# Kernel optimization log

Hardware: AMD Instinct MI355X
Metric: run time of the kernel (lower is better)

## Reference

```python
import jax, jax.numpy as jnp
import numpy as np

N_EMBED = 1024
N_HEAD = 16


def setup_inputs() -> dict:
    key = jax.random.key(0)
    k1, k2, k3 = jax.random.split(key, 3)
    B, T, C = 4, 2048, N_EMBED
    x = jax.random.normal(k1, (B, T, C), dtype=jnp.float32)
    # Linear weights stored as [in, out] so forward is x @ W
    scale = 1.0 / np.sqrt(C)
    W_attn = jax.random.normal(k2, (C, 3 * C), dtype=jnp.float32) * scale
    W_proj = jax.random.normal(k3, (C, C), dtype=jnp.float32) * scale
    return {"x": x, "W_attn": W_attn, "W_proj": W_proj}


def reference(x, W_attn, W_proj):
    B, T, C = x.shape
    H = N_HEAD
    D = C // H
    qkv = x @ W_attn  # [B, T, 3C]
    q, k, v = jnp.split(qkv, 3, axis=-1)
    # [B, H, T, D]
    q = q.reshape(B, T, H, D).transpose(0, 2, 1, 3)
    k = k.reshape(B, T, H, D).transpose(0, 2, 1, 3)
    v = v.reshape(B, T, H, D).transpose(0, 2, 1, 3)
    scores = jnp.einsum('bhqd,bhkd->bhqk', q, k) * (1.0 / np.sqrt(D))
    causal = jnp.tril(jnp.ones((T, T), dtype=bool))
    scores = jnp.where(causal, scores, -jnp.inf)
    attn = jax.nn.softmax(scores, axis=-1)
    y = jnp.einsum('bhqk,bhkd->bhqd', attn, v)  # [B, H, T, D]
    y = y.transpose(0, 2, 1, 3).reshape(B, T, C)
    return y @ W_proj
```

## Files before the change

kernel.cpp:

```cpp
#include <hip/hip_runtime.h>

using bf16x8 = __attribute__((ext_vector_type(8))) __bf16;
using f32x4  = __attribute__((ext_vector_type(4))) float;
using f32x16 = __attribute__((ext_vector_type(16))) float;

__device__ __forceinline__ unsigned short f2bf(float f) {
  unsigned u = __builtin_bit_cast(unsigned, f);
  u += 0x7fffu + ((u >> 16) & 1u);
  return (unsigned short)(u >> 16);
}

__device__ __forceinline__ unsigned cvt_pk_bf16(float lo, float hi) {
  unsigned r;
  asm("v_cvt_pk_bf16_f32 %0, %1, %2" : "=v"(r) : "v"(lo), "v"(hi));
  return r;
}

__device__ __forceinline__ void permswap(unsigned &a, unsigned &b) {
  asm("v_permlane32_swap_b32 %0, %1" : "+v"(a), "+v"(b));
}

__device__ __forceinline__ void gload_lds16(const void* g, void* l) {
  __builtin_amdgcn_global_load_lds((const __attribute__((address_space(1))) void*)g,
                                   (__attribute__((address_space(3))) void*)l, 16, 0, 0);
}

__global__ void prep_kernel(const float* __restrict__ x, unsigned short* __restrict__ xb,
                            const float* __restrict__ Wa, unsigned short* __restrict__ WaT,
                            const float* __restrict__ Wp, unsigned short* __restrict__ WpT) {
  __shared__ float tile[32][33];
  const int bid = blockIdx.x;
  const int tid = threadIdx.x;
  if (bid < 8192) {
    int i = (bid * 256 + tid) * 4;
    float4 f = *(const float4*)(x + i);
    ushort4 o;
    o.x = f2bf(f.x); o.y = f2bf(f.y); o.z = f2bf(f.z); o.w = f2bf(f.w);
    *(ushort4*)(xb + i) = o;
    return;
  }
  const float* W; unsigned short* WT; int N, tb;
  if (bid < 11264) { W = Wa; WT = WaT; N = 3072; tb = bid - 8192; }
  else             { W = Wp; WT = WpT; N = 1024; tb = bid - 11264; }
  const int nt = N >> 5;
  const int n0 = (tb % nt) * 32, k0 = (tb / nt) * 32;
  const int tx = tid & 31, ty = tid >> 5;
  #pragma unroll
  for (int i = 0; i < 32; i += 8)
    tile[ty + i][tx] = W[(size_t)(k0 + ty + i) * N + (n0 + tx)];
  __syncthreads();
  #pragma unroll
  for (int i = 0; i < 32; i += 8)
    WT[(size_t)(n0 + ty + i) * 1024 + (k0 + tx)] = f2bf(tile[tx][ty + i]);
}

template <int MODE>
__global__ __launch_bounds__(256, 2)
void gemm_bf16(const unsigned short* __restrict__ A,
               const unsigned short* __restrict__ BT,
               float* __restrict__ Cout, int K,
               unsigned short* __restrict__ q_out,
               unsigned short* __restrict__ k_out,
               unsigned short* __restrict__ v_out, int N) {
  __shared__ alignas(16) char smem[32768];
  char* As = smem;
  char* Bs = smem + 16384;
  const int tid = threadIdx.x;
  const int lane = tid & 63, w = tid >> 6;
  const int wm = w >> 1, wn = w & 1;
  const int l15 = lane & 15, l4 = lane >> 4;
  const int bm = blockIdx.y, bn = blockIdx.x;

  f32x4 acc[4][4] = {};

  for (int kt = 0; kt < K; kt += 64) {
    #pragma unroll
    for (int i = 0; i < 4; i++) {
      int row = i * 32 + w * 8 + (lane >> 3);
      int sc = (lane & 7) ^ (row & 7);
      gload_lds16(A + (size_t)(bm * 128 + row) * K + kt + sc * 8, As + i * 4096 + w * 1024);
      gload_lds16(BT + (size_t)(bn * 128 + row) * K + kt + sc * 8, Bs + i * 4096 + w * 1024);
    }
    __syncthreads();
    #pragma unroll
    for (int kk = 0; kk < 2; kk++) {
      bf16x8 af[4], bfr[4];
      #pragma unroll
      for (int mc = 0; mc < 4; mc++) {
        int row = wm * 64 + mc * 16 + l15;
        af[mc] = *(const bf16x8*)(As + row * 128 + (((kk * 4 + l4) ^ (row & 7)) << 4));
      }
      #pragma unroll
      for (int nc = 0; nc < 4; nc++) {
        int row = wn * 64 + nc * 16 + l15;
        bfr[nc] = *(const bf16x8*)(Bs + row * 128 + (((kk * 4 + l4) ^ (row & 7)) << 4));
      }
      #pragma unroll
      for (int mc = 0; mc < 4; mc++)
        #pragma unroll
        for (int nc = 0; nc < 4; nc++)
          acc[mc][nc] = __builtin_amdgcn_mfma_f32_16x16x32_bf16(af[mc], bfr[nc], acc[mc][nc], 0, 0, 0);
    }
    __syncthreads();
  }

  if (MODE == 0 && bn >= 16) {
    unsigned short* tt = (unsigned short*)smem;
    #pragma unroll
    for (int mc = 0; mc < 4; mc++)
      #pragma unroll
      for (int nc = 0; nc < 4; nc++)
        #pragma unroll
        for (int r = 0; r < 4; r++) {
          int ml = wm * 64 + mc * 16 + l4 * 4 + r;
          int nl = wn * 64 + nc * 16 + l15;
          tt[nl * 128 + (ml ^ ((nl & 7) << 3))] = f2bf(acc[mc][nc][r]);
        }
    __syncthreads();
    const int b_ = bm >> 4;
    const int t0 = (bm & 15) * 128;
    const int mm = (tid & 15) * 8;
    #pragma unroll
    for (int it = 0; it < 8; it++) {
      int nl = it * 16 + (tid >> 4);
      int n = bn * 128 + nl;
      int h = (n >> 6) & 15, d = n & 63;
      int4 val = *(const int4*)&tt[nl * 128 + (mm ^ ((nl & 7) << 3))];
      *(int4*)(v_out + ((size_t)(b_ * 16 + h) * 64 + d) * 2048 + t0 + mm) = val;
    }
  } else {
    const float qsc = (MODE == 0 && bn < 8) ? 0.18033688f : 1.0f;
    #pragma unroll
    for (int mc = 0; mc < 4; mc++) {
      #pragma unroll
      for (int nc = 0; nc < 4; nc++) {
        #pragma unroll
        for (int r = 0; r < 4; r++) {
          int m = bm * 128 + wm * 64 + mc * 16 + l4 * 4 + r;
          int n = bn * 128 + wn * 64 + nc * 16 + l15;
          float val = acc[mc][nc][r] * qsc;
          if (MODE == 0) {
            int b = m >> 11, t = m & 2047;
            int which = n >> 10, h = (n >> 6) & 15, d = n & 63;
            unsigned short* dst = (which == 0) ? q_out : k_out;
            dst[(((size_t)(b * 16 + h)) * 2048 + t) * 64 + d] = f2bf(val);
          } else {
            Cout[(size_t)m * N + n] = val;
          }
        }
      }
    }
  }
}

__device__ __forceinline__ void repack_pa(const f32x16 s, bf16x8 &fl, bf16x8 &fh) {
  unsigned p01 = cvt_pk_bf16(s[0], s[1]);
  unsigned p23 = cvt_pk_bf16(s[2], s[3]);
  unsigned p45 = cvt_pk_bf16(s[4], s[5]);
  unsigned p67 = cvt_pk_bf16(s[6], s[7]);
  unsigned p89 = cvt_pk_bf16(s[8], s[9]);
  unsigned pAB = cvt_pk_bf16(s[10], s[11]);
  unsigned pCD = cvt_pk_bf16(s[12], s[13]);
  unsigned pEF = cvt_pk_bf16(s[14], s[15]);
  permswap(p01, p45);
  permswap(p23, p67);
  permswap(p89, pCD);
  permswap(pAB, pEF);
  uint4 f0, f1;
  f0.x = p01; f0.y = p23; f0.z = p45; f0.w = p67;
  f1.x = p89; f1.y = pAB; f1.z = pCD; f1.w = pEF;
  fl = __builtin_bit_cast(bf16x8, f0);
  fh = __builtin_bit_cast(bf16x8, f1);
}

__global__ __launch_bounds__(256, 4)
void attn_kernel(const unsigned short* __restrict__ q,
                 const unsigned short* __restrict__ k,
                 const unsigned short* __restrict__ vT,
                 unsigned short* __restrict__ att) {
  __shared__ alignas(16) char smem[32768];

  const int bid = blockIdx.x;
  const int qt = 15 - (bid >> 6);
  const int bh = bid & 63;
  const int tid = threadIdx.x;
  const int lane = tid & 63, w = tid >> 6;
  const int l31 = lane & 31, hi = lane >> 5;
  const size_t base = (size_t)bh * 2048 * 64;

  bf16x8 qf[4];
  const int qwb = qt * 128 + w * 32;
  const int qrow = qwb + l31;
  #pragma unroll
  for (int ks = 0; ks < 4; ks++)
    qf[ks] = *(const bf16x8*)(q + base + (size_t)qrow * 64 + ks * 16 + hi * 8);
  asm volatile("" :: "v"(qf[0]), "v"(qf[1]), "v"(qf[2]), "v"(qf[3]));

  const char* kb4[4];
  #pragma unroll
  for (int ks = 0; ks < 4; ks++)
    kb4[ks] = smem + l31 * 128 + (((2 * ks + hi) ^ (l31 & 7)) << 4);

  const int srow = w * 8 + (lane >> 3);
  const int sc8 = ((lane & 7) ^ (srow & 7)) * 8;

  f32x16 o0 = {}, o1 = {}, lacc = {};
  const int qmax = qwb + 31;
  const int ntiles = 2 * qt + 2;

  uint4 onesw;
  onesw.x = 0x3F803F80u; onesw.y = 0x3F803F80u; onesw.z = 0x3F803F80u; onesw.w = 0x3F803F80u;
  const bf16x8 onesv = __builtin_bit_cast(bf16x8, onesw);

  {
    const unsigned short* kp = k + base + srow * 64 + sc8;
    gload_lds16(kp,         smem + w * 1024);
    gload_lds16(kp + 2048,  smem + 4096 + w * 1024);
    const unsigned short* vp = vT + base + (size_t)srow * 2048 + sc8;
    gload_lds16(vp,          smem + 16384 + w * 1024);
    gload_lds16(vp + 65536,  smem + 16384 + 4096 + w * 1024);
  }
  const unsigned short* kq1 = k + base + srow * 64 + sc8 + 4096;
  const unsigned short* kq2 = kq1 + 4096;
  const unsigned short* vq1 = vT + base + (size_t)srow * 2048 + sc8 + 64;
  const unsigned short* vq2 = vq1 + 64;

#define COMPUTE_TILE(BUF, KBASE)                                               \
  do {                                                                         \
    const int kbase_ = (KBASE);                                                \
    if (kbase_ <= qmax) {                                                      \
      f32x16 s0 = {}, s1 = {};                                                 \
      __builtin_amdgcn_s_setprio(1);                                           \
      _Pragma("unroll")                                                        \
      for (int ks = 0; ks < 4; ks++) {                                         \
        bf16x8 k0 = *(const bf16x8*)(kb4[ks] + (BUF));                         \
        bf16x8 k1 = *(const bf16x8*)(kb4[ks] + (BUF) + 4096);                  \
        s0 = __builtin_amdgcn_mfma_f32_32x32x16_bf16(k0, qf[ks], s0, 0, 0, 0); \
        s1 = __builtin_amdgcn_mfma_f32_32x32x16_bf16(k1, qf[ks], s1, 0, 0, 0); \
      }                                                                        \
      __builtin_amdgcn_s_setprio(0);                                           \
      if (kbase_ + 63 > qwb) {                                                 \
        _Pragma("unroll")                                                      \
        for (int r = 0; r < 16; r++) {                                         \
          int crow = (r & 3) + 8 * (r >> 2) + 4 * hi;                          \
          if (kbase_ + crow > qrow) s0[r] = -1e30f;                            \
          if (kbase_ + 32 + crow > qrow) s1[r] = -1e30f;                       \
        }                                                                      \
      }                                                                        \
      _Pragma("unroll")                                                        \
      for (int r = 0; r < 16; r++) {                                           \
        float t0_ = s0[r], t1_ = s1[r];                                        \
        asm("v_exp_f32 %0, %0" : "+v"(t0_));                                   \
        asm("v_exp_f32 %0, %0" : "+v"(t1_));                                   \
        s0[r] = t0_; s1[r] = t1_;                                              \
      }                                                                        \
      bf16x8 pa[4];                                                            \
      repack_pa(s0, pa[0], pa[1]);                                             \
      repack_pa(s1, pa[2], pa[3]);                                             \
      __builtin_amdgcn_s_setprio(1);                                           \
      _Pragma("unroll")                                                        \
      for (int ks = 0; ks < 4; ks++) {                                         \
        bf16x8 vf0 = *(const bf16x8*)(kb4[ks] + 16384 + (BUF));                \
        bf16x8 vf1 = *(const bf16x8*)(kb4[ks] + 16384 + (BUF) + 4096);         \
        o0 = __builtin_amdgcn_mfma_f32_32x32x16_bf16(pa[ks], vf0, o0, 0, 0, 0);\
        o1 = __builtin_amdgcn_mfma_f32_32x32x16_bf16(pa[ks], vf1, o1, 0, 0, 0);\
        lacc = __builtin_amdgcn_mfma_f32_32x32x16_bf16(pa[ks], onesv, lacc, 0, 0, 0);\
      }                                                                        \
      __builtin_amdgcn_s_setprio(0);                                           \
    }                                                                          \
  } while (0)

  for (int t = 0; t < ntiles; t += 2) {
    gload_lds16(kq1,         smem + 8192 + w * 1024);
    gload_lds16(kq1 + 2048,  smem + 8192 + 4096 + w * 1024);
    gload_lds16(vq1,         smem + 16384 + 8192 + w * 1024);
    gload_lds16(vq1 + 65536, smem + 16384 + 8192 + 4096 + w * 1024);
    kq1 += 8192; vq1 += 128;
    asm volatile("s_waitcnt vmcnt(4)" ::: "memory");
    __builtin_amdgcn_s_barrier();
    __builtin_amdgcn_sched_barrier(0);
    COMPUTE_TILE(0, t * 64);
    __builtin_amdgcn_s_barrier();
    __builtin_amdgcn_sched_barrier(0);

    if (t + 2 < ntiles) {
      gload_lds16(kq2,         smem + w * 1024);
      gload_lds16(kq2 + 2048,  smem + 4096 + w * 1024);
      gload_lds16(vq2,         smem + 16384 + w * 1024);
      gload_lds16(vq2 + 65536, smem + 16384 + 4096 + w * 1024);
      kq2 += 8192; vq2 += 128;
      asm volatile("s_waitcnt vmcnt(4)" ::: "memory");
    } else {
      asm volatile("s_waitcnt vmcnt(0)" ::: "memory");
    }
    __builtin_amdgcn_s_barrier();
    __builtin_amdgcn_sched_barrier(0);
    COMPUTE_TILE(8192, t * 64 + 64);
    __builtin_amdgcn_s_barrier();
    __builtin_amdgcn_sched_barrier(0);
  }
#undef COMPUTE_TILE

  const int b_ = bh >> 4, h = bh & 15;
  #pragma unroll
  for (int r = 0; r < 16; r++) {
    int crow = (r & 3) + 8 * (r >> 2) + 4 * hi;
    float li = 1.0f / lacc[r];
    int t = qt * 128 + w * 32 + crow;
    size_t rb = ((size_t)(b_ * 2048 + t)) * 1024 + h * 64;
    att[rb + l31] = f2bf(o0[r] * li);
    att[rb + 32 + l31] = f2bf(o1[r] * li);
  }
}

extern "C" void kernel_launch(void* const* d_in, const int* in_sizes, int n_in,
                              void* d_out, int out_size, void* d_ws, size_t ws_size,
                              hipStream_t stream) {
  const float* x  = (const float*)d_in[0];
  const float* Wa = (const float*)d_in[1];
  const float* Wp = (const float*)d_in[2];
  float* out = (float*)d_out;
  char* ws = (char*)d_ws;

  unsigned short* xb  = (unsigned short*)(ws);
  unsigned short* WaT = (unsigned short*)(ws + 16777216);
  unsigned short* WpT = (unsigned short*)(ws + 23068672);
  unsigned short* qb  = (unsigned short*)(ws + 25165824);
  unsigned short* kb  = (unsigned short*)(ws + 41943040);
  unsigned short* vtb = (unsigned short*)(ws + 58720256);
  unsigned short* att = xb;

  prep_kernel<<<12288, 256, 0, stream>>>(x, xb, Wa, WaT, Wp, WpT);

  gemm_bf16<0><<<dim3(24, 64), 256, 0, stream>>>(xb, WaT, nullptr, 1024, qb, kb, vtb, 3072);

  attn_kernel<<<1024, 256, 0, stream>>>(qb, kb, vtb, att);

  gemm_bf16<1><<<dim3(8, 64), 256, 0, stream>>>(att, WpT, out, 1024, nullptr, nullptr, nullptr, 1024);
}
```

Before: 148.0 us.

## Rewrite GEMMs as 256x128 double-buffered tiles with async LDS prefetch

Replaces the 128x128 single-buffered bf16 GEMM with a 256x128 tile using 512 threads, a 96KB double-buffered LDS ring, and global_load_lds prefetch of the next K-slice interleaved with MFMA work under s_setprio. The goal is to hide global-load latency behind the matrix math and to improve operand reuse per block. In exchange, occupancy drops to one block per CU, and the output projection runs only 256 blocks, which may underfill the GPU.

```diff
diff --git a/kernel.cpp b/kernel.cpp
--- a/kernel.cpp
+++ b/kernel.cpp
@@ -55,100 +55,152 @@
 }
 
 template <int MODE>
-__global__ __launch_bounds__(256, 2)
-void gemm_bf16(const unsigned short* __restrict__ A,
-               const unsigned short* __restrict__ BT,
-               float* __restrict__ Cout, int K,
-               unsigned short* __restrict__ q_out,
-               unsigned short* __restrict__ k_out,
-               unsigned short* __restrict__ v_out, int N) {
-  __shared__ alignas(16) char smem[32768];
-  char* As = smem;
-  char* Bs = smem + 16384;
+__global__ __launch_bounds__(512, 1)
+void gemm256x128(const unsigned short* __restrict__ A,
+                 const unsigned short* __restrict__ BT,
+                 float* __restrict__ Cout,
+                 unsigned short* __restrict__ q_out,
+                 unsigned short* __restrict__ k_out,
+                 unsigned short* __restrict__ v_out) {
+  constexpr int K = 1024;
+  __shared__ alignas(16) char smem[98304];
+
   const int tid = threadIdx.x;
   const int lane = tid & 63, w = tid >> 6;
   const int wm = w >> 1, wn = w & 1;
   const int l15 = lane & 15, l4 = lane >> 4;
   const int bm = blockIdx.y, bn = blockIdx.x;
 
+  const int srow = tid >> 3;
+  const int schunk = ((tid & 7) ^ (srow & 7)) * 8;
+  const unsigned short* pa = A + (size_t)(bm * 256 + srow) * K + schunk;
+  const unsigned short* pb = BT + (size_t)(bn * 128 + srow) * K + schunk;
+  const int sdst = w * 1024;
+
   f32x4 acc[4][4] = {};
 
-  for (int kt = 0; kt < K; kt += 64) {
-    #pragma unroll
-    for (int i = 0; i < 4; i++) {
-      int row = i * 32 + w * 8 + (lane >> 3);
-      int sc = (lane & 7) ^ (row & 7);
-      gload_lds16(A + (size_t)(bm * 128 + row) * K + kt + sc * 8, As + i * 4096 + w * 1024);
-      gload_lds16(BT + (size_t)(bn * 128 + row) * K + kt + sc * 8, Bs + i * 4096 + w * 1024);
-    }
-    __syncthreads();
-    #pragma unroll
-    for (int kk = 0; kk < 2; kk++) {
-      bf16x8 af[4], bfr[4];
-      #pragma unroll
-      for (int mc = 0; mc < 4; mc++) {
-        int row = wm * 64 + mc * 16 + l15;
-        af[mc] = *(const bf16x8*)(As + row * 128 + (((kk * 4 + l4) ^ (row & 7)) << 4));
-      }
-      #pragma unroll
-      for (int nc = 0; nc < 4; nc++) {
-        int row = wn * 64 + nc * 16 + l15;
-        bfr[nc] = *(const bf16x8*)(Bs + row * 128 + (((kk * 4 + l4) ^ (row & 7)) << 4));
-      }
-      #pragma unroll
-      for (int mc = 0; mc < 4; mc++)
-        #pragma unroll
-        for (int nc = 0; nc < 4; nc++)
-          acc[mc][nc] = __builtin_amdgcn_mfma_f32_16x16x32_bf16(af[mc], bfr[nc], acc[mc][nc], 0, 0, 0);
-    }
-    __syncthreads();
-  }
-
-  if (MODE == 0 && bn >= 16) {
-    unsigned short* tt = (unsigned short*)smem;
-    #pragma unroll
-    for (int mc = 0; mc < 4; mc++)
-      #pragma unroll
-      for (int nc = 0; nc < 4; nc++)
+#define GLA(j, buf, tcol) gload_lds16(pa + (size_t)(j) * 64 * K + (tcol), \
+                                      smem + (buf) * 32768 + (j) * 8192 + sdst)
+#define GLB(j, buf, tcol) gload_lds16(pb + (size_t)(j) * 64 * K + (tcol), \
+                                      smem + 65536 + (buf) * 16384 + (j) * 8192 + sdst)
+
+  GLA(0, 0, 0); GLA(1, 0, 0); GLA(2, 0, 0); GLA(3, 0, 0);
+  GLB(0, 0, 0); GLB(1, 0, 0);
+
+  for (int t = 0; t < 16; t++) {
+    const int cur = t & 1, nxt = cur ^ 1;
+    const int tcol = (t + 1) * 64;
+    const bool more = (t < 15);
+
+    __builtin_amdgcn_s_barrier();
+    if (more) { GLA(0, nxt, tcol); GLA(1, nxt, tcol); }
+    if (more) asm volatile("s_waitcnt vmcnt(2)" ::: "memory");
+    else      asm volatile("s_waitcnt vmcnt(0)" ::: "memory");
+    __builtin_amdgcn_s_barrier();
+    __builtin_amdgcn_sched_barrier(0);
+
+    const char* Ab = smem + cur * 32768;
+    const char* Bb = smem + 65536 + cur * 16384;
+
+    bf16x8 bf[4][2];
+    #pragma unroll
+    for (int nf = 0; nf < 4; nf++) {
+      int rowb = wn * 64 + nf * 16 + l15;
+      #pragma unroll
+      for (int kc = 0; kc < 2; kc++)
+        bf[nf][kc] = *(const bf16x8*)(Bb + rowb * 128 + (((kc * 4 + l4) ^ (rowb & 7)) << 4));
+    }
+    bf16x8 a0[2][2], a1[2][2];
+    #pragma unroll
+    for (int i = 0; i < 2; i++) {
+      int rowa = wm * 64 + i * 16 + l15;
+      #pragma unroll
+      for (int kc = 0; kc < 2; kc++)
+        a0[i][kc] = *(const bf16x8*)(Ab + rowa * 128 + (((kc * 4 + l4) ^ (rowa & 7)) << 4));
+    }
+
+#define LDA(dst, mfb)                                                            \
+    _Pragma("unroll")                                                            \
+    for (int i = 0; i < 2; i++) {                                                \
+      int rowa = wm * 64 + ((mfb) + i) * 16 + l15;                               \
+      _Pragma("unroll")                                                          \
+      for (int kc = 0; kc < 2; kc++)                                             \
+        dst[i][kc] = *(const bf16x8*)(Ab + rowa * 128 + (((kc * 4 + l4) ^ (rowa & 7)) << 4)); \
+    }
+#define MFMA16(mb, af)                                                           \
+    __builtin_amdgcn_s_setprio(1);                                               \
+    _Pragma("unroll")                                                            \
+    for (int m = 0; m < 2; m++)                                                  \
+      _Pragma("unroll")                                                          \
+      for (int nf = 0; nf < 4; nf++) {                                           \
+        acc[(mb) + m][nf] = __builtin_amdgcn_mfma_f32_16x16x32_bf16(af[m][0], bf[nf][0], acc[(mb) + m][nf], 0, 0, 0); \
+        acc[(mb) + m][nf] = __builtin_amdgcn_mfma_f32_16x16x32_bf16(af[m][1], bf[nf][1], acc[(mb) + m][nf], 0, 0, 0); \
+      }                                                                          \
+    __builtin_amdgcn_s_setprio(0);                                               \
+    __builtin_amdgcn_sched_barrier(0);
+
+    LDA(a1, 2);
+    if (more) { GLA(2, nxt, tcol); GLA(3, nxt, tcol); GLB(0, nxt, tcol); GLB(1, nxt, tcol); }
+    MFMA16(0, a0);
+    MFMA16(2, a1);
+#undef LDA
+#undef MFMA16
+  }
+#undef GLA
+#undef GLB
+
+  if (MODE == 1) {
+    #pragma unroll
+    for (int mf = 0; mf < 4; mf++)
+      #pragma unroll
+      for (int nf = 0; nf < 4; nf++)
         #pragma unroll
         for (int r = 0; r < 4; r++) {
-          int ml = wm * 64 + mc * 16 + l4 * 4 + r;
-          int nl = wn * 64 + nc * 16 + l15;
-          tt[nl * 128 + (ml ^ ((nl & 7) << 3))] = f2bf(acc[mc][nc][r]);
+          int m = bm * 256 + wm * 64 + mf * 16 + l4 * 4 + r;
+          int n = bn * 128 + wn * 64 + nf * 16 + l15;
+          Cout[(size_t)m * 1024 + n] = acc[mf][nf][r];
+        }
+  } else if (bn < 16) {
+    const float qsc = (bn < 8) ? 0.18033688f : 1.0f;
+    unsigned short* dst = (bn < 8) ? q_out : k_out;
+    #pragma unroll
+    for (int mf = 0; mf < 4; mf++) {
+      #pragma unroll
+      for (int nf = 0; nf < 4; nf++) {
+        #pragma unroll
+        for (int r = 0; r < 4; r++) {
+          int m = bm * 256 + wm * 64 + mf * 16 + l4 * 4 + r;
+          int n = bn * 128 + wn * 64 + nf * 16 + l15;
+          int h = (n >> 6) & 15, d = n & 63;
+          dst[((size_t)((m >> 11) * 16 + h) * 2048 + (m & 2047)) * 64 + d] =
+              f2bf(acc[mf][nf][r] * qsc);
+        }
+      }
+    }
+  } else {
+    __syncthreads();
+    unsigned short* tt = (unsigned short*)smem;
+    #pragma unroll
+    for (int mf = 0; mf < 4; mf++)
+      #pragma unroll
+      for (int nf = 0; nf < 4; nf++)
+        #pragma unroll
+        for (int r = 0; r < 4; r++) {
+          int row_l = wm * 64 + mf * 16 + l4 * 4 + r;
+          int cl = wn * 64 + nf * 16 + l15;
+          tt[cl * 256 + (row_l ^ ((cl & 7) << 3))] = f2bf(acc[mf][nf][r]);
         }
     __syncthreads();
-    const int b_ = bm >> 4;
-    const int t0 = (bm & 15) * 128;
-    const int mm = (tid & 15) * 8;
-    #pragma unroll
-    for (int it = 0; it < 8; it++) {
-      int nl = it * 16 + (tid >> 4);
-      int n = bn * 128 + nl;
-      int h = (n >> 6) & 15, d = n & 63;
-      int4 val = *(const int4*)&tt[nl * 128 + (mm ^ ((nl & 7) << 3))];
+    const int b_ = bm >> 3;
+    const int t0 = (bm & 7) * 256;
+    const int mm = (tid & 31) * 8;
+    #pragma unroll
+    for (int p = 0; p < 8; p++) {
+      int cl = p * 16 + (tid >> 5);
+      int4 val = *(const int4*)&tt[cl * 256 + (mm ^ ((cl & 7) << 3))];
+      int vh = (bn - 16) * 128 + cl;
+      int h = vh >> 6, d = vh & 63;
       *(int4*)(v_out + ((size_t)(b_ * 16 + h) * 64 + d) * 2048 + t0 + mm) = val;
-    }
-  } else {
-    const float qsc = (MODE == 0 && bn < 8) ? 0.18033688f : 1.0f;
-    #pragma unroll
-    for (int mc = 0; mc < 4; mc++) {
-      #pragma unroll
-      for (int nc = 0; nc < 4; nc++) {
-        #pragma unroll
-        for (int r = 0; r < 4; r++) {
-          int m = bm * 128 + wm * 64 + mc * 16 + l4 * 4 + r;
-          int n = bn * 128 + wn * 64 + nc * 16 + l15;
-          float val = acc[mc][nc][r] * qsc;
-          if (MODE == 0) {
-            int b = m >> 11, t = m & 2047;
-            int which = n >> 10, h = (n >> 6) & 15, d = n & 63;
-            unsigned short* dst = (which == 0) ? q_out : k_out;
-            dst[(((size_t)(b * 16 + h)) * 2048 + t) * 64 + d] = f2bf(val);
-          } else {
-            Cout[(size_t)m * N + n] = val;
-          }
-        }
-      }
     }
   }
 }
@@ -332,9 +384,9 @@
 
   prep_kernel<<<12288, 256, 0, stream>>>(x, xb, Wa, WaT, Wp, WpT);
 
-  gemm_bf16<0><<<dim3(24, 64), 256, 0, stream>>>(xb, WaT, nullptr, 1024, qb, kb, vtb, 3072);
+  gemm256x128<0><<<dim3(24, 32), 512, 0, stream>>>(xb, WaT, nullptr, qb, kb, vtb);
 
   attn_kernel<<<1024, 256, 0, stream>>>(qb, kb, vtb, att);
 
-  gemm_bf16<1><<<dim3(8, 64), 256, 0, stream>>>(att, WpT, out, 1024, nullptr, nullptr, nullptr, 1024);
-}
+  gemm256x128<1><<<dim3(8, 32), 512, 0, stream>>>(att, WpT, out, nullptr, nullptr, nullptr);
+}
```

New measurement: 149.9 us. No clear change (+1.3%).

## Give each attention wave 64 query rows, halving waves per block

Applied to the files above, without the earlier changes.

The attention block drops from four waves of 32 query rows to two waves of 64 query rows each. Each K and V fragment read from LDS is now reused across two query sub-tiles, and each wave issues twice as many async global-to-LDS loads per stage. The aim is to cut LDS read traffic and barrier participants per unit of MFMA work. In exchange, register pressure roughly doubles for accumulators and Q fragments, and occupancy drops.

```diff
diff --git a/kernel.cpp b/kernel.cpp
--- a/kernel.cpp
+++ b/kernel.cpp
@@ -173,7 +173,7 @@
   fh = __builtin_bit_cast(bf16x8, f1);
 }
 
-__global__ __launch_bounds__(256, 4)
+__global__ __launch_bounds__(128, 2)
 void attn_kernel(const unsigned short* __restrict__ q,
                  const unsigned short* __restrict__ k,
                  const unsigned short* __restrict__ vT,
@@ -188,24 +188,26 @@
   const int l31 = lane & 31, hi = lane >> 5;
   const size_t base = (size_t)bh * 2048 * 64;
 
-  bf16x8 qf[4];
-  const int qwb = qt * 128 + w * 32;
-  const int qrow = qwb + l31;
-  #pragma unroll
-  for (int ks = 0; ks < 4; ks++)
-    qf[ks] = *(const bf16x8*)(q + base + (size_t)qrow * 64 + ks * 16 + hi * 8);
-  asm volatile("" :: "v"(qf[0]), "v"(qf[1]), "v"(qf[2]), "v"(qf[3]));
+  const int qwb = qt * 128 + w * 64;
+  bf16x8 qf0[4], qf1[4];
+  #pragma unroll
+  for (int ks = 0; ks < 4; ks++) {
+    qf0[ks] = *(const bf16x8*)(q + base + (size_t)(qwb + l31) * 64 + ks * 16 + hi * 8);
+    qf1[ks] = *(const bf16x8*)(q + base + (size_t)(qwb + 32 + l31) * 64 + ks * 16 + hi * 8);
+  }
+  asm volatile("" :: "v"(qf0[0]), "v"(qf0[1]), "v"(qf0[2]), "v"(qf0[3]),
+                     "v"(qf1[0]), "v"(qf1[1]), "v"(qf1[2]), "v"(qf1[3]));
 
   const char* kb4[4];
   #pragma unroll
   for (int ks = 0; ks < 4; ks++)
     kb4[ks] = smem + l31 * 128 + (((2 * ks + hi) ^ (l31 & 7)) << 4);
 
-  const int srow = w * 8 + (lane >> 3);
-  const int sc8 = ((lane & 7) ^ (srow & 7)) * 8;
-
-  f32x16 o0 = {}, o1 = {}, lacc = {};
-  const int qmax = qwb + 31;
+  const int srow8 = w * 8 + (lane >> 3);
+  const int sc8 = ((lane & 7) ^ (srow8 & 7)) * 8;
+
+  f32x16 o00 = {}, o01 = {}, o10 = {}, o11 = {}, lacc0 = {}, lacc1 = {};
+  const int qmax = qwb + 63;
   const int ntiles = 2 * qt + 2;
 
   uint4 onesw;
@@ -213,70 +215,119 @@
   const bf16x8 onesv = __builtin_bit_cast(bf16x8, onesw);
 
   {
-    const unsigned short* kp = k + base + srow * 64 + sc8;
-    gload_lds16(kp,         smem + w * 1024);
-    gload_lds16(kp + 2048,  smem + 4096 + w * 1024);
-    const unsigned short* vp = vT + base + (size_t)srow * 2048 + sc8;
-    gload_lds16(vp,          smem + 16384 + w * 1024);
-    gload_lds16(vp + 65536,  smem + 16384 + 4096 + w * 1024);
-  }
-  const unsigned short* kq1 = k + base + srow * 64 + sc8 + 4096;
+    const unsigned short* kp = k + base + (size_t)srow8 * 64 + sc8;
+    const unsigned short* vp = vT + base + (size_t)srow8 * 2048 + sc8;
+    #pragma unroll
+    for (int j = 0; j < 4; j++) {
+      gload_lds16(kp + j * 1024,  smem + j * 2048 + w * 1024);
+      gload_lds16(vp + j * 32768, smem + 16384 + j * 2048 + w * 1024);
+    }
+  }
+  const unsigned short* kq1 = k + base + (size_t)srow8 * 64 + sc8 + 4096;
   const unsigned short* kq2 = kq1 + 4096;
-  const unsigned short* vq1 = vT + base + (size_t)srow * 2048 + sc8 + 64;
+  const unsigned short* vq1 = vT + base + (size_t)srow8 * 2048 + sc8 + 64;
   const unsigned short* vq2 = vq1 + 64;
+
+#define STAGE(BUF, KP, VP)                                                     \
+  do {                                                                         \
+    _Pragma("unroll")                                                          \
+    for (int j = 0; j < 4; j++) {                                              \
+      gload_lds16((KP) + j * 1024,  smem + (BUF) + j * 2048 + w * 1024);       \
+      gload_lds16((VP) + j * 32768, smem + 16384 + (BUF) + j * 2048 + w * 1024);\
+    }                                                                          \
+  } while (0)
 
 #define COMPUTE_TILE(BUF, KBASE)                                               \
   do {                                                                         \
     const int kbase_ = (KBASE);                                                \
     if (kbase_ <= qmax) {                                                      \
-      f32x16 s0 = {}, s1 = {};                                                 \
-      __builtin_amdgcn_s_setprio(1);                                           \
+                                    \
+      bf16x8 kf[4][2];                                                         \
       _Pragma("unroll")                                                        \
       for (int ks = 0; ks < 4; ks++) {                                         \
-        bf16x8 k0 = *(const bf16x8*)(kb4[ks] + (BUF));                         \
-        bf16x8 k1 = *(const bf16x8*)(kb4[ks] + (BUF) + 4096);                  \
-        s0 = __builtin_amdgcn_mfma_f32_32x32x16_bf16(k0, qf[ks], s0, 0, 0, 0); \
-        s1 = __builtin_amdgcn_mfma_f32_32x32x16_bf16(k1, qf[ks], s1, 0, 0, 0); \
+        kf[ks][0] = *(const bf16x8*)(kb4[ks] + (BUF));                         \
+        kf[ks][1] = *(const bf16x8*)(kb4[ks] + (BUF) + 4096);                  \
       }                                                                        \
-      __builtin_amdgcn_s_setprio(0);                                           \
-      if (kbase_ + 63 > qwb) {                                                 \
+      bf16x8 pa0[4], pa1[4];                                                   \
+                                                        \
+      {                                                                        \
+        f32x16 s0 = {}, s1 = {};                                               \
+        __builtin_amdgcn_s_setprio(1);                                         \
+        _Pragma("unroll")                                                      \
+        for (int ks = 0; ks < 4; ks++) {                                       \
+          s0 = __builtin_amdgcn_mfma_f32_32x32x16_bf16(kf[ks][0], qf0[ks], s0, 0, 0, 0); \
+          s1 = __builtin_amdgcn_mfma_f32_32x32x16_bf16(kf[ks][1], qf0[ks], s1, 0, 0, 0); \
+        }                                                                      \
+        __builtin_amdgcn_s_setprio(0);                                         \
+        const int qrow_ = qwb + l31;                                           \
+        if (kbase_ + 63 > qwb) {                                               \
+          _Pragma("unroll")                                                    \
+          for (int r = 0; r < 16; r++) {                                       \
+            int crow = (r & 3) + 8 * (r >> 2) + 4 * hi;                        \
+            if (kbase_ + crow > qrow_) s0[r] = -1e30f;                         \
+            if (kbase_ + 32 + crow > qrow_) s1[r] = -1e30f;                    \
+          }                                                                    \
+        }                                                                      \
         _Pragma("unroll")                                                      \
         for (int r = 0; r < 16; r++) {                                         \
-          int crow = (r & 3) + 8 * (r >> 2) + 4 * hi;                          \
-          if (kbase_ + crow > qrow) s0[r] = -1e30f;                            \
-          if (kbase_ + 32 + crow > qrow) s1[r] = -1e30f;                       \
-        }                                                                      \
+          float t0_ = s0[r], t1_ = s1[r];                                      \
+          asm("v_exp_f32 %0, %0" : "+v"(t0_));                                 \
+          asm("v_exp_f32 %0, %0" : "+v"(t1_));                                 \
+          s0[r] = t0_; s1[r] = t1_;                                            \
+        }                                                                      \
+        repack_pa(s0, pa0[0], pa0[1]);                                         \
+        repack_pa(s1, pa0[2], pa0[3]);                                         \
       }                                                                        \
-      _Pragma("unroll")                                                        \
-      for (int r = 0; r < 16; r++) {                                           \
-        float t0_ = s0[r], t1_ = s1[r];                                        \
-        asm("v_exp_f32 %0, %0" : "+v"(t0_));                                   \
-        asm("v_exp_f32 %0, %0" : "+v"(t1_));                                   \
-        s0[r] = t0_; s1[r] = t1_;                                              \
+                                                        \
+      {                                                                        \
+        f32x16 s0 = {}, s1 = {};                                               \
+        __builtin_amdgcn_s_setprio(1);                                         \
+        _Pragma("unroll")                                                      \
+        for (int ks = 0; ks < 4; ks++) {                                       \
+          s0 = __builtin_amdgcn_mfma_f32_32x32x16_bf16(kf[ks][0], qf1[ks], s0, 0, 0, 0); \
+          s1 = __builtin_amdgcn_mfma_f32_32x32x16_bf16(kf[ks][1], qf1[ks], s1, 0, 0, 0); \
+        }                                                                      \
+        __builtin_amdgcn_s_setprio(0);                                         \
+        const int qrow_ = qwb + 32 + l31;                                      \
+        if (kbase_ + 63 > qwb + 32) {                                          \
+          _Pragma("unroll")                                                    \
+          for (int r = 0; r < 16; r++) {                                       \
+            int crow = (r & 3) + 8 * (r >> 2) + 4 * hi;                        \
+            if (kbase_ + crow > qrow_) s0[r] = -1e30f;                         \
+            if (kbase_ + 32 + crow > qrow_) s1[r] = -1e30f;                    \
+          }                                                                    \
+        }                                                                      \
+        _Pragma("unroll")                                                      \
+        for (int r = 0; r < 16; r++) {                                         \
+          float t0_ = s0[r], t1_ = s1[r];                                      \
+          asm("v_exp_f32 %0, %0" : "+v"(t0_));                                 \
+          asm("v_exp_f32 %0, %0" : "+v"(t1_));                                 \
+          s0[r] = t0_; s1[r] = t1_;                                            \
+        }                                                                      \
+        repack_pa(s0, pa1[0], pa1[1]);                                         \
+        repack_pa(s1, pa1[2], pa1[3]);                                         \
       }                                                                        \
-      bf16x8 pa[4];                                                            \
-      repack_pa(s0, pa[0], pa[1]);                                             \
-      repack_pa(s1, pa[2], pa[3]);                                             \
+                              \
       __builtin_amdgcn_s_setprio(1);                                           \
       _Pragma("unroll")                                                        \
       for (int ks = 0; ks < 4; ks++) {                                         \
         bf16x8 vf0 = *(const bf16x8*)(kb4[ks] + 16384 + (BUF));                \
         bf16x8 vf1 = *(const bf16x8*)(kb4[ks] + 16384 + (BUF) + 4096);         \
-        o0 = __builtin_amdgcn_mfma_f32_32x32x16_bf16(pa[ks], vf0, o0, 0, 0, 0);\
-        o1 = __builtin_amdgcn_mfma_f32_32x32x16_bf16(pa[ks], vf1, o1, 0, 0, 0);\
-        lacc = __builtin_amdgcn_mfma_f32_32x32x16_bf16(pa[ks], onesv, lacc, 0, 0, 0);\
+        o00 = __builtin_amdgcn_mfma_f32_32x32x16_bf16(pa0[ks], vf0, o00, 0, 0, 0); \
+        o01 = __builtin_amdgcn_mfma_f32_32x32x16_bf16(pa0[ks], vf1, o01, 0, 0, 0); \
+        o10 = __builtin_amdgcn_mfma_f32_32x32x16_bf16(pa1[ks], vf0, o10, 0, 0, 0); \
+        o11 = __builtin_amdgcn_mfma_f32_32x32x16_bf16(pa1[ks], vf1, o11, 0, 0, 0); \
+        lacc0 = __builtin_amdgcn_mfma_f32_32x32x16_bf16(pa0[ks], onesv, lacc0, 0, 0, 0); \
+        lacc1 = __builtin_amdgcn_mfma_f32_32x32x16_bf16(pa1[ks], onesv, lacc1, 0, 0, 0); \
       }                                                                        \
       __builtin_amdgcn_s_setprio(0);                                           \
     }                                                                          \
   } while (0)
 
   for (int t = 0; t < ntiles; t += 2) {
-    gload_lds16(kq1,         smem + 8192 + w * 1024);
-    gload_lds16(kq1 + 2048,  smem + 8192 + 4096 + w * 1024);
-    gload_lds16(vq1,         smem + 16384 + 8192 + w * 1024);
-    gload_lds16(vq1 + 65536, smem + 16384 + 8192 + 4096 + w * 1024);
+    STAGE(8192, kq1, vq1);
     kq1 += 8192; vq1 += 128;
-    asm volatile("s_waitcnt vmcnt(4)" ::: "memory");
+    asm volatile("s_waitcnt vmcnt(8)" ::: "memory");
     __builtin_amdgcn_s_barrier();
     __builtin_amdgcn_sched_barrier(0);
     COMPUTE_TILE(0, t * 64);
@@ -284,12 +335,9 @@
     __builtin_amdgcn_sched_barrier(0);
 
     if (t + 2 < ntiles) {
-      gload_lds16(kq2,         smem + w * 1024);
-      gload_lds16(kq2 + 2048,  smem + 4096 + w * 1024);
-      gload_lds16(vq2,         smem + 16384 + w * 1024);
-      gload_lds16(vq2 + 65536, smem + 16384 + 4096 + w * 1024);
+      STAGE(0, kq2, vq2);
       kq2 += 8192; vq2 += 128;
-      asm volatile("s_waitcnt vmcnt(4)" ::: "memory");
+      asm volatile("s_waitcnt vmcnt(8)" ::: "memory");
     } else {
       asm volatile("s_waitcnt vmcnt(0)" ::: "memory");
     }
@@ -300,16 +348,26 @@
     __builtin_amdgcn_sched_barrier(0);
   }
 #undef COMPUTE_TILE
+#undef STAGE
 
   const int b_ = bh >> 4, h = bh & 15;
   #pragma unroll
   for (int r = 0; r < 16; r++) {
     int crow = (r & 3) + 8 * (r >> 2) + 4 * hi;
-    float li = 1.0f / lacc[r];
-    int t = qt * 128 + w * 32 + crow;
-    size_t rb = ((size_t)(b_ * 2048 + t)) * 1024 + h * 64;
-    att[rb + l31] = f2bf(o0[r] * li);
-    att[rb + 32 + l31] = f2bf(o1[r] * li);
+    {
+      float li = 1.0f / lacc0[r];
+      int t = qwb + crow;
+      size_t rb = ((size_t)(b_ * 2048 + t)) * 1024 + h * 64;
+      att[rb + l31] = f2bf(o00[r] * li);
+      att[rb + 32 + l31] = f2bf(o01[r] * li);
+    }
+    {
+      float li = 1.0f / lacc1[r];
+      int t = qwb + 32 + crow;
+      size_t rb = ((size_t)(b_ * 2048 + t)) * 1024 + h * 64;
+      att[rb + l31] = f2bf(o10[r] * li);
+      att[rb + 32 + l31] = f2bf(o11[r] * li);
+    }
   }
 }
 
@@ -334,7 +392,7 @@
 
   gemm_bf16<0><<<dim3(24, 64), 256, 0, stream>>>(xb, WaT, nullptr, 1024, qb, kb, vtb, 3072);
 
-  attn_kernel<<<1024, 256, 0, stream>>>(qb, kb, vtb, att);
+  attn_kernel<<<1024, 128, 0, stream>>>(qb, kb, vtb, att);
 
   gemm_bf16<1><<<dim3(8, 64), 256, 0, stream>>>(att, WpT, out, 1024, nullptr, nullptr, nullptr, 1024);
 }
```

Result: slower. 170.6 us (+15.3%).
